# Performance work log

Hardware: AMD Instinct MI355X
Metric: run time of the kernel (lower is better)

The kernel has to match this reference:

```python
import jax, jax.numpy as jnp
import numpy as np

N = 400_000   # active voxels
C = 128       # inplanes = outplanes
K = 9         # nplanes*3*3 kernel offsets (nplanes=1)
EPS = 1e-4    # scn BatchNormalization default eps


def setup_inputs() -> dict:
    key = jax.random.key(0)
    ks = jax.random.split(key, 5)
    feat = jax.random.normal(ks[0], (N, C), dtype=jnp.float32)
    # rulebook: neighbor active-site index per kernel offset, plus validity mask
    nbr_idx = jax.random.randint(ks[1], (N, K), 0, N, dtype=jnp.int32)
    nbr_idx = nbr_idx.at[:, K // 2].set(jnp.arange(N, dtype=jnp.int32))  # center = self
    nbr_mask = jax.random.uniform(ks[2], (N, K)) < 0.6
    nbr_mask = nbr_mask.at[:, K // 2].set(True)
    scale = 1.0 / np.sqrt(K * C)
    W1 = jax.random.normal(ks[3], (K, C, C), dtype=jnp.float32) * scale
    W2 = jax.random.normal(ks[4], (K, C, C), dtype=jnp.float32) * scale
    gamma1 = jnp.ones((C,), jnp.float32)
    beta1 = jnp.zeros((C,), jnp.float32)
    gamma2 = jnp.ones((C,), jnp.float32)
    beta2 = jnp.zeros((C,), jnp.float32)
    return {"feat": feat, "W1": W1, "W2": W2,
            "gamma1": gamma1, "beta1": beta1,
            "gamma2": gamma2, "beta2": beta2,
            "nbr_idx": nbr_idx, "nbr_mask": nbr_mask}


def _subm_conv(feat, nbr_idx, nbr_mask, W):
    # rulebook gather -> GEMM -> accumulate; output lives at the same active sites
    out = jnp.zeros((feat.shape[0], W.shape[2]), feat.dtype)
    for k in range(W.shape[0]):  # small fixed K=9 structural loop
        xk = jnp.where(nbr_mask[:, k:k + 1], feat[nbr_idx[:, k]], 0.0)
        out = out + xk @ W[k]
    return out


def _batchnorm(x, gamma, beta):
    mu = jnp.mean(x, axis=0)
    var = jnp.mean(jnp.square(x - mu), axis=0)
    return (x - mu) * (gamma * jax.lax.rsqrt(var + EPS)) + beta


def reference(feat, W1, W2, gamma1, beta1, gamma2, beta2, nbr_idx, nbr_mask):
    residual = feat                                   # scn.Identity (stride=1)
    out = _subm_conv(feat, nbr_idx, nbr_mask, W1)     # conv1
    out = jax.nn.relu(_batchnorm(out, gamma1, beta1))  # BatchNormReLU
    out = _subm_conv(out, nbr_idx, nbr_mask, W2)      # conv2
    out = _batchnorm(out, gamma2, beta2)              # bn2
    return jax.nn.relu(out + residual)                # AddTable + ReLU
```

## Files before the change

kernel.cpp:

```cpp
#include <hip/hip_runtime.h>


#define C_CH 128
#define K_OFF 9
#define MTILE 128

typedef __attribute__((ext_vector_type(8))) short bf16x8;
typedef __attribute__((ext_vector_type(4))) float f32x4;
typedef __attribute__((ext_vector_type(8))) unsigned short u16x8;

typedef __attribute__((address_space(1))) const unsigned int* gas_p;
typedef __attribute__((address_space(3))) unsigned int* las_p;

__device__ __forceinline__ void gload_lds16(const unsigned short* g, unsigned short* l) {
    __builtin_amdgcn_global_load_lds((gas_p)g, (las_p)l, 16, 0, 0);
}

__device__ __forceinline__ unsigned short f2b(float f) {
    union { float f; unsigned u; } v; v.f = f;
    unsigned r = v.u + 0x7fffu + ((v.u >> 16) & 1u);
    return (unsigned short)(r >> 16);
}
__device__ __forceinline__ float b2f(unsigned short h) {
    union { unsigned u; float f; } v; v.u = ((unsigned)h) << 16;
    return v.f;
}


__global__ void init_detect_k(float* stats, unsigned int* zrow1, unsigned int* zrow2,
                              const unsigned char* __restrict__ m, int* flagA, int* flagB) {
    int t = threadIdx.x;
    if (blockIdx.x == 0) {
        if (t < 256) { stats[t] = 0.f; stats[256 + t] = 0.f; }
        if (t >= 256 && t < 258) ((int*)stats)[1024 + (t - 256)] = 0;
        if (t < 64) { zrow1[t] = 0u; zrow2[t] = 0u; }
    } else {
        int i = (blockIdx.x - 1) * 256 + t;
        unsigned char v = m[i];
        if ((i & 3) != 0 && v != 0) atomicOr(flagA, 1);
        if (v > 1) atomicOr(flagB, 1);
    }
}

__global__ void prep_k(const float* __restrict__ x, unsigned short* __restrict__ y, int n4,
                       const float* __restrict__ W1, unsigned short* __restrict__ Wp1,
                       const float* __restrict__ W2, unsigned short* __restrict__ Wp2,
                       const int* __restrict__ nidx, const void* __restrict__ m,
                       const int* __restrict__ flagA, const int* __restrict__ flagB,
                       int* __restrict__ eidx, int NK, int N) {
    const int PACK = K_OFF * 8 * 4 * 512;
    int fa = *flagA, fb = *flagB;
    int i = blockIdx.x * blockDim.x + threadIdx.x;
    int s = gridDim.x * blockDim.x;
    int tot = n4 + 2 * PACK + NK;
    for (; i < tot; i += s) {
        if (i < n4) {
            float4 f = ((const float4*)x)[i];
            ushort4 o;
            o.x = f2b(f.x); o.y = f2b(f.y); o.z = f2b(f.z); o.w = f2b(f.w);
            ((ushort4*)y)[i] = o;
        } else if (i < n4 + 2 * PACK) {
            int ii = i - n4;
            const float* W = (ii < PACK) ? W1 : W2;
            unsigned short* Wp = (ii < PACK) ? Wp1 : Wp2;
            if (ii >= PACK) ii -= PACK;
            int j = ii & 7;
            int l = (ii >> 3) & 63;
            int frag = ii >> 9;
            int ks = frag & 3;
            int nt = (frag >> 2) & 7;
            int ko = frag >> 5;
            int cin = ks * 32 + (l >> 4) * 8 + j;
            int cout = nt * 16 + (l & 15);
            Wp[ii] = f2b(W[ko * C_CH * C_CH + cin * C_CH + cout]);
        } else {
            int j = i - n4 - 2 * PACK;
            bool t;
            if (!fa)       t = ((const int*)m)[j] != 0;
            else if (fb)   t = ((const unsigned*)m)[j] != 0;
            else           t = ((const unsigned char*)m)[j] != 0;
            eidx[j] = t ? nidx[j] : N;
        }
    }
}


__global__ __launch_bounds__(512) void conv_kernel(
    const unsigned short* __restrict__ Xb,
    const unsigned short* __restrict__ Wp,
    const int* __restrict__ eidx,
    unsigned short* __restrict__ Yraw,
    float* __restrict__ statS, float* __restrict__ statQ)
{
    const int tid = threadIdx.x;
    const int lane = tid & 63;
    const int wv = tid >> 6;
    const int wr = wv >> 2;
    const int wc = wv & 3;
    const int tile = blockIdx.x * MTILE;
    const int asub = lane >> 4;
    const int l15 = lane & 15;

    __shared__ alignas(16) unsigned short At[2][MTILE * C_CH];
    __shared__ int sIdxT[K_OFF][MTILE];

    for (int i = tid; i < MTILE * K_OFF; i += 512) {
        int r = i / K_OFF, k = i - r * K_OFF;
        sIdxT[k][r] = eidx[(size_t)(tile + r) * K_OFF + k];
    }
    __syncthreads();

    const int r_st = tid >> 4;
    const int ch_st = tid & 15;

    #define STAGE(buf, ko)                                                        \
        {                                                                         \
            _Pragma("unroll")                                                     \
            for (int jr = 0; jr < 4; ++jr) {                                      \
                int r = jr * 32 + r_st;                                           \
                int g = sIdxT[ko][r];                                             \
                const unsigned short* src =                                       \
                    Xb + (size_t)g * C_CH + ((ch_st ^ (r & 7)) * 8);              \
                unsigned short* dst = &At[buf][r * C_CH + ch_st * 8];             \
                gload_lds16(src, dst);                                            \
            }                                                                     \
        }

    f32x4 acc[4][2];
    #pragma unroll
    for (int m = 0; m < 4; ++m) { acc[m][0] = (f32x4){0,0,0,0}; acc[m][1] = (f32x4){0,0,0,0}; }

    STAGE(0, 0);

    #define CONV_ITER(KO)                                                         \
        {                                                                         \
            bf16x8 bfrag0[4], bfrag1[4];                                          \
            const unsigned short* wb = Wp + (size_t)(KO) * (8 * 4 * 512) + lane * 8; \
            _Pragma("unroll")                                                     \
            for (int ks = 0; ks < 4; ++ks) {                                      \
                bfrag0[ks] = *(const bf16x8*)(wb + ((wc * 2 + 0) * 4 + ks) * 512);\
                bfrag1[ks] = *(const bf16x8*)(wb + ((wc * 2 + 1) * 4 + ks) * 512);\
            }                                                                     \
            __builtin_amdgcn_sched_barrier(0);                                    \
            asm volatile("s_waitcnt vmcnt(8)" ::: "memory");                      \
            __builtin_amdgcn_s_barrier();                                         \
            __builtin_amdgcn_sched_barrier(0);                                    \
            if ((KO) + 1 < K_OFF) { STAGE((((KO) + 1) & 1), (KO) + 1); }          \
            __builtin_amdgcn_s_setprio(1);                                        \
            _Pragma("unroll")                                                     \
            for (int m = 0; m < 4; ++m) {                                         \
                bf16x8 a[4];                                                      \
                _Pragma("unroll")                                                 \
                for (int ks = 0; ks < 4; ++ks) {                                  \
                    int row = wr * 64 + m * 16 + l15;                             \
                    int sc = (ks * 4 + asub) ^ (row & 7);                         \
                    a[ks] = *(const bf16x8*)((const char*)At[(KO) & 1] + row * 256 + sc * 16); \
                }                                                                 \
                _Pragma("unroll")                                                 \
                for (int ks = 0; ks < 4; ++ks) {                                  \
                    acc[m][0] = __builtin_amdgcn_mfma_f32_16x16x32_bf16(a[ks], bfrag0[ks], acc[m][0], 0, 0, 0); \
                    acc[m][1] = __builtin_amdgcn_mfma_f32_16x16x32_bf16(a[ks], bfrag1[ks], acc[m][1], 0, 0, 0); \
                }                                                                 \
            }                                                                     \
            __builtin_amdgcn_s_setprio(0);                                        \
        }

    CONV_ITER(0)
    CONV_ITER(1)
    CONV_ITER(2)
    CONV_ITER(3)
    CONV_ITER(4)
    CONV_ITER(5)
    CONV_ITER(6)
    CONV_ITER(7)
    CONV_ITER(8)
    #undef CONV_ITER
    #undef STAGE

    #pragma unroll
    for (int j = 0; j < 2; ++j) {
        float s = 0.f, q = 0.f;
        #pragma unroll
        for (int m = 0; m < 4; ++m)
            #pragma unroll
            for (int r = 0; r < 4; ++r) { float v = acc[m][j][r]; s += v; q += v * v; }
        s += __shfl_xor(s, 16); s += __shfl_xor(s, 32);
        q += __shfl_xor(q, 16); q += __shfl_xor(q, 32);
        if (lane < 16) {
            atomicAdd(&statS[wc * 32 + j * 16 + lane], s);
            atomicAdd(&statQ[wc * 32 + j * 16 + lane], q);
        }
    }

    #pragma unroll
    for (int m = 0; m < 4; ++m)
        #pragma unroll
        for (int j = 0; j < 2; ++j) {
            int col = (wc * 2 + j) * 16 + l15;
            #pragma unroll
            for (int r = 0; r < 4; ++r) {
                int row = tile + wr * 64 + m * 16 + asub * 4 + r;
                Yraw[(size_t)row * C_CH + col] = f2b(acc[m][j][r]);
            }
        }
}


__global__ void finalize_bn_k(const float* __restrict__ S, const float* __restrict__ Q,
                              const float* __restrict__ gamma, const float* __restrict__ beta,
                              float* __restrict__ scale, float* __restrict__ bias, float invN) {
    int c = threadIdx.x;
    if (c < C_CH) {
        float mu = S[c] * invN;
        float var = Q[c] * invN - mu * mu;
        float inv = rsqrtf(var + 1e-4f);
        float sc = gamma[c] * inv;
        scale[c] = sc;
        bias[c] = beta[c] - mu * sc;
    }
}

__global__ void bn_relu_k(unsigned short* __restrict__ y,
                          const float* __restrict__ scale, const float* __restrict__ bias, int n8) {
    int i0 = blockIdx.x * blockDim.x + threadIdx.x;
    int S = gridDim.x * blockDim.x;
    int c0 = (i0 * 8) & (C_CH - 1);
    float sc[8], bs[8];
    #pragma unroll
    for (int j = 0; j < 8; ++j) { sc[j] = scale[c0 + j]; bs[j] = bias[c0 + j]; }
    for (int i = i0; i < n8; i += S) {
        u16x8 v = ((const u16x8*)y)[i];
        #pragma unroll
        for (int j = 0; j < 8; ++j) {
            float x = b2f((unsigned short)v[j]);
            x = fmaxf(x * sc[j] + bs[j], 0.f);
            v[j] = (short)f2b(x);
        }
        ((u16x8*)y)[i] = v;
    }
}

__global__ void final_fuse_k(const unsigned short* __restrict__ raw,
                             const float* __restrict__ feat,
                             const float* __restrict__ scale, const float* __restrict__ bias,
                             float* __restrict__ out, int n4) {
    int i0 = blockIdx.x * blockDim.x + threadIdx.x;
    int S = gridDim.x * blockDim.x;
    int c0 = (i0 * 4) & (C_CH - 1);
    float sc[4], bs[4];
    #pragma unroll
    for (int j = 0; j < 4; ++j) { sc[j] = scale[c0 + j]; bs[j] = bias[c0 + j]; }
    for (int i = i0; i < n4; i += S) {
        ushort4 r = ((const ushort4*)raw)[i];
        float4 f = ((const float4*)feat)[i];
        float4 o;
        o.x = fmaxf(b2f(r.x) * sc[0] + bs[0] + f.x, 0.f);
        o.y = fmaxf(b2f(r.y) * sc[1] + bs[1] + f.y, 0.f);
        o.z = fmaxf(b2f(r.z) * sc[2] + bs[2] + f.z, 0.f);
        o.w = fmaxf(b2f(r.w) * sc[3] + bs[3] + f.w, 0.f);
        ((float4*)out)[i] = o;
    }
}


extern "C" void kernel_launch(void* const* d_in, const int* in_sizes, int n_in,
                              void* d_out, int out_size, void* d_ws, size_t ws_size,
                              hipStream_t stream) {
    const float* feat = (const float*)d_in[0];
    const float* W1 = (const float*)d_in[1];
    const float* W2 = (const float*)d_in[2];
    const float* g1 = (const float*)d_in[3];
    const float* b1 = (const float*)d_in[4];
    const float* g2 = (const float*)d_in[5];
    const float* b2 = (const float*)d_in[6];
    const int* nidx = (const int*)d_in[7];
    const void* nmask = d_in[8];

    const int N = in_sizes[0] / C_CH;
    const int NK = N * K_OFF;

    char* ws = (char*)d_ws;
    unsigned short* featb = (unsigned short*)ws;
    size_t off = (size_t)(N + 1) * C_CH * 2;
    off = (off + 255) & ~(size_t)255;
    unsigned short* Wp1 = (unsigned short*)(ws + off); off += (size_t)K_OFF * C_CH * C_CH * 2;
    unsigned short* Wp2 = (unsigned short*)(ws + off); off += (size_t)K_OFF * C_CH * C_CH * 2;
    float* stats = (float*)(ws + off);
    float* S1 = stats;        float* Q1 = stats + 128;
    float* S2 = stats + 256;  float* Q2 = stats + 384;
    float* sc1 = stats + 512; float* bi1 = stats + 640;
    float* sc2 = stats + 768; float* bi2 = stats + 896;
    int* flagA = ((int*)stats) + 1024;
    int* flagB = ((int*)stats) + 1025;

    unsigned short* y1 = (unsigned short*)d_out;
    int* eidx = (int*)((char*)d_out + (size_t)134217728);
    unsigned short* out2raw = featb;

    hipLaunchKernelGGL(init_detect_k, dim3(65), dim3(256), 0, stream,
                       stats, (unsigned int*)(featb + (size_t)N * C_CH),
                       (unsigned int*)(y1 + (size_t)N * C_CH),
                       (const unsigned char*)nmask, flagA, flagB);
    hipLaunchKernelGGL(prep_k, dim3(2048), dim3(256), 0, stream,
                       feat, featb, N * C_CH / 4,
                       W1, Wp1, W2, Wp2,
                       nidx, nmask, flagA, flagB, eidx, NK, N);

    hipLaunchKernelGGL(conv_kernel, dim3(N / MTILE), dim3(512), 0, stream,
                       featb, Wp1, eidx, y1, S1, Q1);
    hipLaunchKernelGGL(finalize_bn_k, dim3(1), dim3(128), 0, stream, S1, Q1, g1, b1, sc1, bi1, 1.0f / N);
    hipLaunchKernelGGL(bn_relu_k, dim3(2048), dim3(256), 0, stream, y1, sc1, bi1, N * C_CH / 8);

    hipLaunchKernelGGL(conv_kernel, dim3(N / MTILE), dim3(512), 0, stream,
                       y1, Wp2, eidx, out2raw, S2, Q2);
    hipLaunchKernelGGL(finalize_bn_k, dim3(1), dim3(128), 0, stream, S2, Q2, g2, b2, sc2, bi2, 1.0f / N);
    hipLaunchKernelGGL(final_fuse_k, dim3(2048), dim3(256), 0, stream,
                       out2raw, feat, sc2, bi2, (float*)d_out, N * C_CH / 4);
}
```

Baseline: 604.9 us.

## Switch conv to 32x32x16 MFMA with 64-row tiles and triple-buffered gathers

Rewrites the gather-GEMM conv kernel to use 32x32x16 bf16 MFMA instead of 16x16x32. The weight pre-pack layout is changed to match. The M tile shrinks from 128 to 64 rows with 256-thread blocks, so each wave now computes a 32x64 output tile. The LDS staging goes from double to triple buffering, prefetching two kernel offsets ahead with adjusted vmcnt waits. The aim is fewer MFMA issues, more blocks in flight and more gather latency hidden. In exchange each block reuses weights across fewer rows, and the hand-tuned wait counts add fragility.

After: 871.1 us. 1.44x slower.

```diff
diff --git a/kernel.cpp b/kernel.cpp
--- a/kernel.cpp
+++ b/kernel.cpp
@@ -3,10 +3,10 @@
 
 #define C_CH 128
 #define K_OFF 9
-#define MTILE 128
+#define MTILE 64
 
 typedef __attribute__((ext_vector_type(8))) short bf16x8;
-typedef __attribute__((ext_vector_type(4))) float f32x4;
+typedef __attribute__((ext_vector_type(16))) float f32x16;
 typedef __attribute__((ext_vector_type(8))) unsigned short u16x8;
 
 typedef __attribute__((address_space(1))) const unsigned int* gas_p;
@@ -48,7 +48,7 @@
                        const int* __restrict__ nidx, const void* __restrict__ m,
                        const int* __restrict__ flagA, const int* __restrict__ flagB,
                        int* __restrict__ eidx, int NK, int N) {
-    const int PACK = K_OFF * 8 * 4 * 512;
+    const int PACK = K_OFF * 4 * 8 * 512;
     int fa = *flagA, fb = *flagB;
     int i = blockIdx.x * blockDim.x + threadIdx.x;
     int s = gridDim.x * blockDim.x;
@@ -67,11 +67,11 @@
             int j = ii & 7;
             int l = (ii >> 3) & 63;
             int frag = ii >> 9;
-            int ks = frag & 3;
-            int nt = (frag >> 2) & 7;
+            int ks = frag & 7;
+            int nt = (frag >> 3) & 3;
             int ko = frag >> 5;
-            int cin = ks * 32 + (l >> 4) * 8 + j;
-            int cout = nt * 16 + (l & 15);
+            int cin = ks * 16 + (l >> 5) * 8 + j;
+            int cout = nt * 32 + (l & 31);
             Wp[ii] = f2b(W[ko * C_CH * C_CH + cin * C_CH + cout]);
         } else {
             int j = i - n4 - 2 * PACK;
@@ -85,7 +85,7 @@
 }
 
 
-__global__ __launch_bounds__(512) void conv_kernel(
+__global__ __launch_bounds__(256) void conv_kernel(
     const unsigned short* __restrict__ Xb,
     const unsigned short* __restrict__ Wp,
     const int* __restrict__ eidx,
@@ -95,16 +95,16 @@
     const int tid = threadIdx.x;
     const int lane = tid & 63;
     const int wv = tid >> 6;
-    const int wr = wv >> 2;
-    const int wc = wv & 3;
+    const int wr = wv >> 1;
+    const int wc = wv & 1;
     const int tile = blockIdx.x * MTILE;
-    const int asub = lane >> 4;
-    const int l15 = lane & 15;
-
-    __shared__ alignas(16) unsigned short At[2][MTILE * C_CH];
+    const int l31 = lane & 31;
+    const int lh = lane >> 5;
+
+    __shared__ alignas(16) unsigned short At[3][MTILE * C_CH];
     __shared__ int sIdxT[K_OFF][MTILE];
 
-    for (int i = tid; i < MTILE * K_OFF; i += 512) {
+    for (int i = tid; i < MTILE * K_OFF; i += 256) {
         int r = i / K_OFF, k = i - r * K_OFF;
         sIdxT[k][r] = eidx[(size_t)(tile + r) * K_OFF + k];
     }
@@ -117,92 +117,91 @@
         {                                                                         \
             _Pragma("unroll")                                                     \
             for (int jr = 0; jr < 4; ++jr) {                                      \
-                int r = jr * 32 + r_st;                                           \
+                int r = jr * 16 + r_st;                                           \
                 int g = sIdxT[ko][r];                                             \
                 const unsigned short* src =                                       \
-                    Xb + (size_t)g * C_CH + ((ch_st ^ (r & 7)) * 8);              \
+                    Xb + (size_t)g * C_CH + ((ch_st ^ (r & 15)) * 8);             \
                 unsigned short* dst = &At[buf][r * C_CH + ch_st * 8];             \
                 gload_lds16(src, dst);                                            \
             }                                                                     \
         }
 
-    f32x4 acc[4][2];
-    #pragma unroll
-    for (int m = 0; m < 4; ++m) { acc[m][0] = (f32x4){0,0,0,0}; acc[m][1] = (f32x4){0,0,0,0}; }
+    f32x16 acc[2];
+    #pragma unroll
+    for (int j = 0; j < 2; ++j)
+        #pragma unroll
+        for (int r = 0; r < 16; ++r) acc[j][r] = 0.f;
 
     STAGE(0, 0);
-
-    #define CONV_ITER(KO)                                                         \
+    STAGE(1, 1);
+
+    #define CONV_ITER(KO, VM)                                                     \
         {                                                                         \
-            bf16x8 bfrag0[4], bfrag1[4];                                          \
-            const unsigned short* wb = Wp + (size_t)(KO) * (8 * 4 * 512) + lane * 8; \
+            bf16x8 bfrag0[8], bfrag1[8];                                          \
+            const unsigned short* wb = Wp + (size_t)(KO) * (4 * 8 * 512) + lane * 8; \
             _Pragma("unroll")                                                     \
-            for (int ks = 0; ks < 4; ++ks) {                                      \
-                bfrag0[ks] = *(const bf16x8*)(wb + ((wc * 2 + 0) * 4 + ks) * 512);\
-                bfrag1[ks] = *(const bf16x8*)(wb + ((wc * 2 + 1) * 4 + ks) * 512);\
+            for (int ks = 0; ks < 8; ++ks) {                                      \
+                bfrag0[ks] = *(const bf16x8*)(wb + ((wc * 2 + 0) * 8 + ks) * 512);\
+                bfrag1[ks] = *(const bf16x8*)(wb + ((wc * 2 + 1) * 8 + ks) * 512);\
             }                                                                     \
             __builtin_amdgcn_sched_barrier(0);                                    \
-            asm volatile("s_waitcnt vmcnt(8)" ::: "memory");                      \
+            asm volatile("s_waitcnt vmcnt(" #VM ")" ::: "memory");                \
             __builtin_amdgcn_s_barrier();                                         \
             __builtin_amdgcn_sched_barrier(0);                                    \
-            if ((KO) + 1 < K_OFF) { STAGE((((KO) + 1) & 1), (KO) + 1); }          \
+            if ((KO) + 2 < K_OFF) { STAGE((((KO) + 2) % 3), (KO) + 2); }          \
             __builtin_amdgcn_s_setprio(1);                                        \
-            _Pragma("unroll")                                                     \
-            for (int m = 0; m < 4; ++m) {                                         \
-                bf16x8 a[4];                                                      \
+            {                                                                     \
+                const int row = wr * 32 + l31;                                    \
+                bf16x8 a[8];                                                      \
                 _Pragma("unroll")                                                 \
-                for (int ks = 0; ks < 4; ++ks) {                                  \
-                    int row = wr * 64 + m * 16 + l15;                             \
-                    int sc = (ks * 4 + asub) ^ (row & 7);                         \
-                    a[ks] = *(const bf16x8*)((const char*)At[(KO) & 1] + row * 256 + sc * 16); \
+                for (int ks = 0; ks < 8; ++ks) {                                  \
+                    int sc = (ks * 2 + lh) ^ (row & 15);                          \
+                    a[ks] = *(const bf16x8*)((const char*)At[(KO) % 3] + row * 256 + sc * 16); \
                 }                                                                 \
                 _Pragma("unroll")                                                 \
-                for (int ks = 0; ks < 4; ++ks) {                                  \
-                    acc[m][0] = __builtin_amdgcn_mfma_f32_16x16x32_bf16(a[ks], bfrag0[ks], acc[m][0], 0, 0, 0); \
-                    acc[m][1] = __builtin_amdgcn_mfma_f32_16x16x32_bf16(a[ks], bfrag1[ks], acc[m][1], 0, 0, 0); \
+                for (int ks = 0; ks < 8; ++ks) {                                  \
+                    acc[0] = __builtin_amdgcn_mfma_f32_32x32x16_bf16(a[ks], bfrag0[ks], acc[0], 0, 0, 0); \
+                    acc[1] = __builtin_amdgcn_mfma_f32_32x32x16_bf16(a[ks], bfrag1[ks], acc[1], 0, 0, 0); \
                 }                                                                 \
             }                                                                     \
             __builtin_amdgcn_s_setprio(0);                                        \
         }
 
-    CONV_ITER(0)
-    CONV_ITER(1)
-    CONV_ITER(2)
-    CONV_ITER(3)
-    CONV_ITER(4)
-    CONV_ITER(5)
-    CONV_ITER(6)
-    CONV_ITER(7)
-    CONV_ITER(8)
+    CONV_ITER(0, 20)
+    CONV_ITER(1, 36)
+    CONV_ITER(2, 36)
+    CONV_ITER(3, 36)
+    CONV_ITER(4, 36)
+    CONV_ITER(5, 36)
+    CONV_ITER(6, 36)
+    CONV_ITER(7, 36)
+    CONV_ITER(8, 32)
     #undef CONV_ITER
     #undef STAGE
 
     #pragma unroll
-    for (int j = 0; j < 2; ++j) {
+    for (int jn = 0; jn < 2; ++jn) {
         float s = 0.f, q = 0.f;
         #pragma unroll
-        for (int m = 0; m < 4; ++m)
-            #pragma unroll
-            for (int r = 0; r < 4; ++r) { float v = acc[m][j][r]; s += v; q += v * v; }
-        s += __shfl_xor(s, 16); s += __shfl_xor(s, 32);
-        q += __shfl_xor(q, 16); q += __shfl_xor(q, 32);
-        if (lane < 16) {
-            atomicAdd(&statS[wc * 32 + j * 16 + lane], s);
-            atomicAdd(&statQ[wc * 32 + j * 16 + lane], q);
-        }
-    }
-
-    #pragma unroll
-    for (int m = 0; m < 4; ++m)
+        for (int r = 0; r < 16; ++r) { float v = acc[jn][r]; s += v; q += v * v; }
+        s += __shfl_xor(s, 32);
+        q += __shfl_xor(q, 32);
+        if (lane < 32) {
+            int col = (wc * 2 + jn) * 32 + l31;
+            atomicAdd(&statS[col], s);
+            atomicAdd(&statQ[col], q);
+        }
+    }
+
+    #pragma unroll
+    for (int jn = 0; jn < 2; ++jn) {
+        int col = (wc * 2 + jn) * 32 + l31;
         #pragma unroll
-        for (int j = 0; j < 2; ++j) {
-            int col = (wc * 2 + j) * 16 + l15;
-            #pragma unroll
-            for (int r = 0; r < 4; ++r) {
-                int row = tile + wr * 64 + m * 16 + asub * 4 + r;
-                Yraw[(size_t)row * C_CH + col] = f2b(acc[m][j][r]);
-            }
-        }
+        for (int r = 0; r < 16; ++r) {
+            int row = tile + wr * 32 + (r & 3) + 8 * (r >> 2) + 4 * lh;
+            Yraw[(size_t)row * C_CH + col] = f2b(acc[jn][r]);
+        }
+    }
 }
 
 
@@ -306,12 +305,12 @@
                        W1, Wp1, W2, Wp2,
                        nidx, nmask, flagA, flagB, eidx, NK, N);
 
-    hipLaunchKernelGGL(conv_kernel, dim3(N / MTILE), dim3(512), 0, stream,
+    hipLaunchKernelGGL(conv_kernel, dim3(N / MTILE), dim3(256), 0, stream,
                        featb, Wp1, eidx, y1, S1, Q1);
     hipLaunchKernelGGL(finalize_bn_k, dim3(1), dim3(128), 0, stream, S1, Q1, g1, b1, sc1, bi1, 1.0f / N);
     hipLaunchKernelGGL(bn_relu_k, dim3(2048), dim3(256), 0, stream, y1, sc1, bi1, N * C_CH / 8);
 
-    hipLaunchKernelGGL(conv_kernel, dim3(N / MTILE), dim3(512), 0, stream,
+    hipLaunchKernelGGL(conv_kernel, dim3(N / MTILE), dim3(256), 0, stream,
                        y1, Wp2, eidx, out2raw, S2, Q2);
     hipLaunchKernelGGL(finalize_bn_k, dim3(1), dim3(128), 0, stream, S2, Q2, g2, b2, sc2, bi2, 1.0f / N);
     hipLaunchKernelGGL(final_fuse_k, dim3(2048), dim3(256), 0, stream,
```

## Shrink conv tile to 64 rows with triple-buffered gather and prefetched weights

Applied to the files above, without the earlier changes.

The sparse conv kernel drops from 128-row tiles with 512 threads to 64-row tiles with 256 threads, aiming for more resident blocks per CU. Each wave now owns a 32-column slice across all 64 rows. The LDS gather buffer goes from double to triple buffering so the gather for offset k+2 is issued while offset k is computed. Weight fragments for the next offset are prefetched into alternating register sets. This hides gather latency better at the cost of more registers, and each weight fragment is now reused over fewer rows.

Result: faster. 565.5 us (-6.5%).

```diff
diff --git a/kernel.cpp b/kernel.cpp
--- a/kernel.cpp
+++ b/kernel.cpp
@@ -3,7 +3,7 @@
 
 #define C_CH 128
 #define K_OFF 9
-#define MTILE 128
+#define MTILE 64
 
 typedef __attribute__((ext_vector_type(8))) short bf16x8;
 typedef __attribute__((ext_vector_type(4))) float f32x4;
@@ -85,7 +85,7 @@
 }
 
 
-__global__ __launch_bounds__(512) void conv_kernel(
+__global__ __launch_bounds__(256, 3) void conv_kernel(
     const unsigned short* __restrict__ Xb,
     const unsigned short* __restrict__ Wp,
     const int* __restrict__ eidx,
@@ -95,16 +95,14 @@
     const int tid = threadIdx.x;
     const int lane = tid & 63;
     const int wv = tid >> 6;
-    const int wr = wv >> 2;
-    const int wc = wv & 3;
     const int tile = blockIdx.x * MTILE;
     const int asub = lane >> 4;
     const int l15 = lane & 15;
 
-    __shared__ alignas(16) unsigned short At[2][MTILE * C_CH];
+    __shared__ alignas(16) unsigned short At[3][MTILE * C_CH];
     __shared__ int sIdxT[K_OFF][MTILE];
 
-    for (int i = tid; i < MTILE * K_OFF; i += 512) {
+    for (int i = tid; i < MTILE * K_OFF; i += 256) {
         int r = i / K_OFF, k = i - r * K_OFF;
         sIdxT[k][r] = eidx[(size_t)(tile + r) * K_OFF + k];
     }
@@ -117,7 +115,7 @@
         {                                                                         \
             _Pragma("unroll")                                                     \
             for (int jr = 0; jr < 4; ++jr) {                                      \
-                int r = jr * 32 + r_st;                                           \
+                int r = jr * 16 + r_st;                                           \
                 int g = sIdxT[ko][r];                                             \
                 const unsigned short* src =                                       \
                     Xb + (size_t)g * C_CH + ((ch_st ^ (r & 7)) * 8);              \
@@ -126,56 +124,75 @@
             }                                                                     \
         }
 
-    f32x4 acc[4][2];
-    #pragma unroll
-    for (int m = 0; m < 4; ++m) { acc[m][0] = (f32x4){0,0,0,0}; acc[m][1] = (f32x4){0,0,0,0}; }
-
-    STAGE(0, 0);
-
-    #define CONV_ITER(KO)                                                         \
+    #define LOADB0(ko)                                                            \
         {                                                                         \
-            bf16x8 bfrag0[4], bfrag1[4];                                          \
-            const unsigned short* wb = Wp + (size_t)(KO) * (8 * 4 * 512) + lane * 8; \
+            const unsigned short* wb = Wp + (size_t)(ko) * (8 * 4 * 512) + lane * 8; \
             _Pragma("unroll")                                                     \
             for (int ks = 0; ks < 4; ++ks) {                                      \
-                bfrag0[ks] = *(const bf16x8*)(wb + ((wc * 2 + 0) * 4 + ks) * 512);\
-                bfrag1[ks] = *(const bf16x8*)(wb + ((wc * 2 + 1) * 4 + ks) * 512);\
+                b0a[ks] = *(const bf16x8*)(wb + ((wv * 2 + 0) * 4 + ks) * 512);   \
+                b0b[ks] = *(const bf16x8*)(wb + ((wv * 2 + 1) * 4 + ks) * 512);   \
             }                                                                     \
+        }
+    #define LOADB1(ko)                                                            \
+        {                                                                         \
+            const unsigned short* wb = Wp + (size_t)(ko) * (8 * 4 * 512) + lane * 8; \
+            _Pragma("unroll")                                                     \
+            for (int ks = 0; ks < 4; ++ks) {                                      \
+                b1a[ks] = *(const bf16x8*)(wb + ((wv * 2 + 0) * 4 + ks) * 512);   \
+                b1b[ks] = *(const bf16x8*)(wb + ((wv * 2 + 1) * 4 + ks) * 512);   \
+            }                                                                     \
+        }
+
+    f32x4 acc[4][2];
+    #pragma unroll
+    for (int m = 0; m < 4; ++m) { acc[m][0] = (f32x4){0,0,0,0}; acc[m][1] = (f32x4){0,0,0,0}; }
+
+    bf16x8 b0a[4], b0b[4], b1a[4], b1b[4];
+
+    STAGE(0, 0);
+    LOADB0(0);
+    STAGE(1, 1);
+
+    #define CONV_ITER(KO, BA, BB, LB, VM)                                         \
+        {                                                                         \
+            if ((KO) + 1 < K_OFF) { LB((KO) + 1); }                               \
             __builtin_amdgcn_sched_barrier(0);                                    \
-            asm volatile("s_waitcnt vmcnt(8)" ::: "memory");                      \
+            asm volatile("s_waitcnt vmcnt(" #VM ")" ::: "memory");                \
             __builtin_amdgcn_s_barrier();                                         \
             __builtin_amdgcn_sched_barrier(0);                                    \
-            if ((KO) + 1 < K_OFF) { STAGE((((KO) + 1) & 1), (KO) + 1); }          \
+            if ((KO) + 2 < K_OFF) { STAGE((((KO) + 2) % 3), (KO) + 2); }          \
             __builtin_amdgcn_s_setprio(1);                                        \
             _Pragma("unroll")                                                     \
             for (int m = 0; m < 4; ++m) {                                         \
                 bf16x8 a[4];                                                      \
                 _Pragma("unroll")                                                 \
                 for (int ks = 0; ks < 4; ++ks) {                                  \
-                    int row = wr * 64 + m * 16 + l15;                             \
+                    int row = m * 16 + l15;                                       \
                     int sc = (ks * 4 + asub) ^ (row & 7);                         \
-                    a[ks] = *(const bf16x8*)((const char*)At[(KO) & 1] + row * 256 + sc * 16); \
+                    a[ks] = *(const bf16x8*)((const char*)At[(KO) % 3] + row * 256 + sc * 16); \
                 }                                                                 \
                 _Pragma("unroll")                                                 \
                 for (int ks = 0; ks < 4; ++ks) {                                  \
-                    acc[m][0] = __builtin_amdgcn_mfma_f32_16x16x32_bf16(a[ks], bfrag0[ks], acc[m][0], 0, 0, 0); \
-                    acc[m][1] = __builtin_amdgcn_mfma_f32_16x16x32_bf16(a[ks], bfrag1[ks], acc[m][1], 0, 0, 0); \
+                    acc[m][0] = __builtin_amdgcn_mfma_f32_16x16x32_bf16(a[ks], BA[ks], acc[m][0], 0, 0, 0); \
+                    acc[m][1] = __builtin_amdgcn_mfma_f32_16x16x32_bf16(a[ks], BB[ks], acc[m][1], 0, 0, 0); \
                 }                                                                 \
             }                                                                     \
             __builtin_amdgcn_s_setprio(0);                                        \
         }
 
-    CONV_ITER(0)
-    CONV_ITER(1)
-    CONV_ITER(2)
-    CONV_ITER(3)
-    CONV_ITER(4)
-    CONV_ITER(5)
-    CONV_ITER(6)
-    CONV_ITER(7)
-    CONV_ITER(8)
+    CONV_ITER(0, b0a, b0b, LOADB1, 12)
+    CONV_ITER(1, b1a, b1b, LOADB0, 12)
+    CONV_ITER(2, b0a, b0b, LOADB1, 12)
+    CONV_ITER(3, b1a, b1b, LOADB0, 12)
+    CONV_ITER(4, b0a, b0b, LOADB1, 12)
+    CONV_ITER(5, b1a, b1b, LOADB0, 12)
+    CONV_ITER(6, b0a, b0b, LOADB1, 12)
+    CONV_ITER(7, b1a, b1b, LOADB0, 12)
+    CONV_ITER(8, b0a, b0b, LOADB1, 0)
     #undef CONV_ITER
     #undef STAGE
+    #undef LOADB0
+    #undef LOADB1
 
     #pragma unroll
     for (int j = 0; j < 2; ++j) {
@@ -187,8 +204,8 @@
         s += __shfl_xor(s, 16); s += __shfl_xor(s, 32);
         q += __shfl_xor(q, 16); q += __shfl_xor(q, 32);
         if (lane < 16) {
-            atomicAdd(&statS[wc * 32 + j * 16 + lane], s);
-            atomicAdd(&statQ[wc * 32 + j * 16 + lane], q);
+            atomicAdd(&statS[wv * 32 + j * 16 + lane], s);
+            atomicAdd(&statQ[wv * 32 + j * 16 + lane], q);
         }
     }
 
@@ -196,10 +213,10 @@
     for (int m = 0; m < 4; ++m)
         #pragma unroll
         for (int j = 0; j < 2; ++j) {
-            int col = (wc * 2 + j) * 16 + l15;
+            int col = (wv * 2 + j) * 16 + l15;
             #pragma unroll
             for (int r = 0; r < 4; ++r) {
-                int row = tile + wr * 64 + m * 16 + asub * 4 + r;
+                int row = tile + m * 16 + asub * 4 + r;
                 Yraw[(size_t)row * C_CH + col] = f2b(acc[m][j][r]);
             }
         }
@@ -306,12 +323,12 @@
                        W1, Wp1, W2, Wp2,
                        nidx, nmask, flagA, flagB, eidx, NK, N);
 
-    hipLaunchKernelGGL(conv_kernel, dim3(N / MTILE), dim3(512), 0, stream,
+    hipLaunchKernelGGL(conv_kernel, dim3(N / MTILE), dim3(256), 0, stream,
                        featb, Wp1, eidx, y1, S1, Q1);
     hipLaunchKernelGGL(finalize_bn_k, dim3(1), dim3(128), 0, stream, S1, Q1, g1, b1, sc1, bi1, 1.0f / N);
     hipLaunchKernelGGL(bn_relu_k, dim3(2048), dim3(256), 0, stream, y1, sc1, bi1, N * C_CH / 8);
 
-    hipLaunchKernelGGL(conv_kernel, dim3(N / MTILE), dim3(512), 0, stream,
+    hipLaunchKernelGGL(conv_kernel, dim3(N / MTILE), dim3(256), 0, stream,
                        y1, Wp2, eidx, out2raw, S2, Q2);
     hipLaunchKernelGGL(finalize_bn_k, dim3(1), dim3(128), 0, stream, S2, Q2, g2, b2, sc2, bi2, 1.0f / N);
     hipLaunchKernelGGL(final_fuse_k, dim3(2048), dim3(256), 0, stream,
```
